# Performance work log

Hardware: AMD Instinct MI355X
Metric: run time of the kernel (lower is better)

Reference implementation:

```python
import jax, jax.numpy as jnp
import numpy as np

L, H, A, NREL2 = 3, 64, 64, 474
N_NODE, N_EDGE, B = 100000, 1000000, 32


def setup_inputs() -> dict:
    key = jax.random.key(0)
    ks = jax.random.split(key, 20)
    f = jax.random.normal
    s = 0.05
    return dict(
        sub_idx=jax.random.randint(ks[0], (N_EDGE,), 0, N_NODE),
        rel_idx=jax.random.randint(ks[1], (N_EDGE,), 0, NREL2),
        obj_idx=jax.random.randint(ks[2], (N_EDGE,), 0, N_NODE),
        edge_batch=jax.random.randint(ks[3], (N_EDGE,), 0, B),
        q_rel=jax.random.randint(ks[4], (B,), 0, NREL2),
        query_sub_idxs=jax.random.randint(ks[5], (B,), 0, N_NODE),
        rela_embed=f(ks[6], (L, NREL2, H)) * s,
        query_rela_embed=f(ks[7], (NREL2, H)) * s,
        Ws=f(ks[8], (L, H, A)) * s,
        Wr=f(ks[9], (L, H, A)) * s,
        Wqr=f(ks[10], (L, H, A)) * s,
        bqr=f(ks[11], (L, A)) * s,
        w_alpha=f(ks[12], (L, A)) * s,
        b_alpha=f(ks[13], (L,)) * s,
        W_h=f(ks[14], (L, H, H)) * s,
        gru_Wih=f(ks[15], (L, 3 * H, H)) * s,
        gru_Whh=f(ks[16], (L, 3 * H, H)) * s,
        gru_bih=f(ks[17], (L, 3 * H)) * s,
        gru_bhh=f(ks[18], (L, 3 * H)) * s,
        W_final=f(ks[19], (H,)) * s,
        n_node=N_NODE,
    )


def reference(sub_idx, rel_idx, obj_idx, edge_batch, q_rel, query_sub_idxs,
              rela_embed, query_rela_embed, Ws, Wr, Wqr, bqr, w_alpha, b_alpha,
              W_h, gru_Wih, gru_Whh, gru_bih, gru_bhh, W_final, n_node):
    # initializer='relation': seed query-subject nodes with query relation embedding
    hidden = jnp.zeros((n_node, H), jnp.float32).at[query_sub_idxs].set(query_rela_embed[q_rel])
    h0 = jnp.zeros((n_node, H), jnp.float32)  # GRU state

    for l in range(L):
        # ---- GNNLayer: gather -> attention MLP -> scatter-add ----
        hs = hidden[sub_idx]                       # [E, H]
        hr = rela_embed[l][rel_idx]                # [E, H]
        h_qr = rela_embed[l][q_rel][edge_batch]    # [E, H] query-rel emb per edge
        pre = jax.nn.relu(hs @ Ws[l] + hr @ Wr[l] + h_qr @ Wqr[l] + bqr[l])  # [E, A]
        alpha = jax.nn.sigmoid(pre @ w_alpha[l] + b_alpha[l])[:, None]       # [E, 1]
        msg = alpha * (hs * hr)                                              # [E, H]
        agg = jax.ops.segment_sum(msg, obj_idx, num_segments=n_node)        # [N, H]
        hidden = jax.nn.relu(agg @ W_h[l])

        # act_signal: mask untouched nodes (detached in original)
        mask = jnp.where(jax.lax.stop_gradient(jnp.sum(hidden, -1)) == 0, 0.0, 1.0)[:, None]

        # ---- one GRU step per node (PyTorch GRU math) ----
        gi = hidden @ gru_Wih[l].T + gru_bih[l]   # [N, 3H]
        gh = h0 @ gru_Whh[l].T + gru_bhh[l]       # [N, 3H]
        i_r, i_z, i_n = jnp.split(gi, 3, axis=-1)
        h_r, h_z, h_n = jnp.split(gh, 3, axis=-1)
        r = jax.nn.sigmoid(i_r + h_r)
        z = jax.nn.sigmoid(i_z + h_z)
        n = jnp.tanh(i_n + r * h_n)
        h_new = (1.0 - z) * n + z * h0
        hidden = h_new * mask
        h0 = h_new * mask

    # readout='linear', no bias
    scores = hidden @ W_final                     # [N]
    return scores
```

## Files before the change

kernel.cpp:

```cpp
#include <hip/hip_runtime.h>
#include <hip/hip_bf16.h>

#define NL 3
#define HD 64
#define TCAP 2048
#define NB 4

typedef unsigned char u8;

__device__ __forceinline__ float sigf(float x){ return 1.f/(1.f+__expf(-x)); }

__device__ __forceinline__ float wsum(float v){
  #pragma unroll
  for (int off=32; off; off>>=1) v += __shfl_xor(v, off, 64);
  return v;
}

__device__ __forceinline__ float bcastf(float v, int l){
  return __int_as_float(__builtin_amdgcn_readlane(__float_as_int(v), l));
}

__device__ __forceinline__ float ldin(const void* p, size_t i, int bf){
  return bf ? __bfloat162float(((const __hip_bfloat16*)p)[i]) : ((const float*)p)[i];
}

__global__ void k_dtype(const unsigned short* __restrict__ probe, int* __restrict__ flag){
  int lane = threadIdx.x & 63;
  unsigned short h = probe[lane];
  int e = (h >> 7) & 0xFF;
  int sane = ((h & 0x7FFF) == 0) || (e >= 96 && e <= 132);
  unsigned long long m = __ballot(sane != 0);
  if (lane == 0) flag[0] = (__popcll(m) >= 56) ? 1 : 0;
}

__global__ void k_prep(
    const void* __restrict__ W_h, const void* __restrict__ Ws,
    const void* __restrict__ Wih, const void* __restrict__ Whh,
    const void* __restrict__ bih, const void* __restrict__ bhh,
    const void* __restrict__ wal, const void* __restrict__ bal,
    const void* __restrict__ Wf,  const void* __restrict__ rel,
    float* __restrict__ WhF, float* __restrict__ WsF,
    float* __restrict__ WiT, float* __restrict__ WhT,
    float* __restrict__ biF, float* __restrict__ bhF,
    float* __restrict__ waF, float* __restrict__ baF,
    float* __restrict__ WfF, float* __restrict__ REL,
    const int* __restrict__ flag, int NR)
{
  int bf = flag[0];
  int j = blockIdx.x*256 + threadIdx.x;
  const int sWT = NL*HD*HD, sWI = NL*192*HD, sB = NL*192;
  if (j < sWT){ WhF[j]=ldin(W_h,j,bf); return; } j-=sWT;
  if (j < sWT){ WsF[j]=ldin(Ws ,j,bf); return; } j-=sWT;
  if (j < sWI){ int l=j/(192*HD), q=j%(192*HD), h=q/192, a=q%192;
                WiT[j]=ldin(Wih,(size_t)l*192*HD + (size_t)a*HD + h,bf); return; } j-=sWI;
  if (j < sWI){ int l=j/(192*HD), q=j%(192*HD), h=q/192, a=q%192;
                WhT[j]=ldin(Whh,(size_t)l*192*HD + (size_t)a*HD + h,bf); return; } j-=sWI;
  if (j < sB){ biF[j]=ldin(bih,j,bf); return; } j-=sB;
  if (j < sB){ bhF[j]=ldin(bhh,j,bf); return; } j-=sB;
  if (j < NL*HD){ waF[j]=ldin(wal,j,bf); return; } j-=NL*HD;
  if (j < NL){ baF[j]=ldin(bal,j,bf); return; } j-=NL;
  if (j < HD){ WfF[j]=ldin(Wf,j,bf); return; } j-=HD;
  if (j < NL*NR*HD){ REL[j]=ldin(rel,j,bf); return; }
}

__global__ void k_tables(
    const void* __restrict__ rel, const void* __restrict__ Wr,
    const void* __restrict__ Wqr, const void* __restrict__ bqr,
    const int* __restrict__ q_rel,
    float* __restrict__ R2, float* __restrict__ QR,
    const int* __restrict__ flag, int NR, int B)
{
  int bf = flag[0];
  int lane = threadIdx.x & 63;
  int bid = blockIdx.x;
  if (bid < NL*NR){
    int l = bid/NR, r = bid%NR;
    float x = ldin(rel,(size_t)(l*NR+r)*HD + lane,bf);
    float acc = 0.f;
    #pragma unroll
    for (int h=0; h<HD; ++h)
      acc = fmaf(bcastf(x, h), ldin(Wr,(size_t)(l*HD+h)*HD + lane,bf), acc);
    R2[(size_t)bid*HD + lane] = acc;
  } else {
    int b2 = bid - NL*NR;
    int l = b2/B, b = b2%B;
    int r = q_rel[b];
    float x = ldin(rel,(size_t)(l*NR+r)*HD + lane,bf);
    float acc = ldin(bqr,(size_t)l*HD + lane,bf);
    #pragma unroll
    for (int h=0; h<HD; ++h)
      acc = fmaf(bcastf(x, h), ldin(Wqr,(size_t)(l*HD+h)*HD + lane,bf), acc);
    QR[(size_t)b2*HD + lane] = acc;
  }
}

__global__ void k_init(
    const int* __restrict__ qsub, const int* __restrict__ q_rel,
    const void* __restrict__ qre, const float* __restrict__ WsF0,
    float* __restrict__ hid, float* __restrict__ HS2, u8* __restrict__ liveB,
    int* __restrict__ stamp, int* __restrict__ plist, int* __restrict__ pcnt,
    const int* __restrict__ flag, int B)
{
  int bf = flag[0];
  int lane = threadIdx.x & 63;
  int b = blockIdx.x;
  int n = qsub[b];
  for (int b2 = b+1; b2 < B; ++b2) if (qsub[b2] == n) return;
  int r = q_rel[b];
  float v = ldin(qre,(size_t)r*HD + lane,bf);
  hid[(size_t)n*HD + lane] = v;
  float acc = 0.f;
  #pragma unroll 8
  for (int h=0; h<HD; ++h)
    acc = fmaf(bcastf(v,h), WsF0[h*HD + lane], acc);
  HS2[(size_t)n*HD + lane] = acc;
  if (lane==0){
    liveB[n] = 1;
    stamp[n] = 1;
    int idx = atomicAdd(pcnt, 1);
    plist[idx] = n;
  }
}

__global__ void __launch_bounds__(256) k_edge(
    const int* __restrict__ sub, const int* __restrict__ rel_i,
    const int* __restrict__ obj, const int* __restrict__ eb,
    const u8* __restrict__ liveB,
    const float* __restrict__ hid, const float* __restrict__ HS2,
    const float* __restrict__ R2l, const float* __restrict__ QRl,
    const float* __restrict__ RELl, const float* __restrict__ waFl,
    const float* __restrict__ baFl, float* __restrict__ agg,
    int* __restrict__ stamp, int* __restrict__ tlist, int* __restrict__ tcnt,
    int ep, int E)
{
  __shared__ int s_cnt;
  __shared__ int s_base;
  __shared__ int s_buf[TCAP];
  if (threadIdx.x == 0) s_cnt = 0;
  __syncthreads();

  int lane = threadIdx.x & 63;
  int wid = (blockIdx.x*256 + threadIdx.x) >> 6;
  int nw = gridDim.x*4;
  float wa = waFl[lane];
  float ba = baFl[0];

  for (long long base = (long long)wid*64; base < E; base += (long long)nw*64){
    int e = (int)base + lane;
    int s = (e < E) ? sub[e] : 0;
    bool liv = (e < E) && (liveB[s] != 0);
    unsigned long long mask = __ballot(liv);
    while (mask){
      int bit = (int)__ffsll(mask) - 1;
      mask &= mask - 1;
      int ee = (int)base + bit;
      int ss = sub[ee], r = rel_i[ee], o = obj[ee], b = eb[ee];
      float hs  = hid[(size_t)ss*HD + lane];
      float pre = HS2[(size_t)ss*HD + lane] + R2l[(size_t)r*HD + lane] + QRl[(size_t)b*HD + lane];
      pre = fmaxf(pre, 0.f);
      float d = wsum(pre*wa) + ba;
      float alpha = sigf(d);
      float msg = alpha * hs * RELl[(size_t)r*HD + lane];
      unsafeAtomicAdd(&agg[(size_t)o*HD + lane], msg);
      if (lane==0){
        int old = atomicExch(&stamp[o], ep);
        if (old != ep){
          int li = atomicAdd(&s_cnt, 1);
          if (li < TCAP) s_buf[li] = o;
          else { int gi = atomicAdd(tcnt, 1); tlist[gi] = o; }
        }
      }
    }
  }

  __syncthreads();
  int cnt = s_cnt; if (cnt > TCAP) cnt = TCAP;
  if (threadIdx.x == 0 && cnt > 0) s_base = atomicAdd(tcnt, cnt);
  __syncthreads();
  if (cnt > 0){
    int b0 = s_base;
    for (int i = threadIdx.x; i < cnt; i += 256) tlist[b0 + i] = s_buf[i];
  }
}

__global__ void __launch_bounds__(256) k_node(
    const int* __restrict__ tlist, const int* __restrict__ tcnt,
    float* __restrict__ agg, float* __restrict__ hid, float* __restrict__ HS2,
    u8* __restrict__ liveB,
    const float* __restrict__ WhFl,
    const float* __restrict__ WiTl,
    const float* __restrict__ WhTl,
    const float* __restrict__ biFl, const float* __restrict__ bhFl,
    const float* __restrict__ WsFn,
    const float* __restrict__ WfF,
    float* __restrict__ out, int N, int isFirst, int isLast)
{
  int cntv = tcnt[0]; if (cntv > N) cntv = N;
  int lane = threadIdx.x & 63;
  int wid = (blockIdx.x*256 + threadIdx.x) >> 6;
  int nw = gridDim.x*4;
  float bi0=biFl[lane], bi1=biFl[HD+lane], bi2=biFl[2*HD+lane];
  float bh0=bhFl[lane], bh1=bhFl[HD+lane], bh2=bhFl[2*HD+lane];
  float wfv = isLast ? WfF[lane] : 0.f;

  for (int i0 = wid*NB; i0 < cntv; i0 += nw*NB){
    int nd[NB]; bool val[NB]; float av[NB];
    #pragma unroll
    for (int j=0;j<NB;++j){
      val[j] = (i0+j) < cntv;
      nd[j]  = tlist[val[j] ? (i0+j) : i0];
      av[j]  = val[j] ? agg[(size_t)nd[j]*HD + lane] : 0.f;
    }
    if (!isLast){
      #pragma unroll
      for (int j=0;j<NB;++j) if (val[j]) agg[(size_t)nd[j]*HD + lane] = 0.f;
    }

    float hm[NB] = {0.f,0.f,0.f,0.f};
    #pragma unroll 8
    for (int h=0; h<HD; ++h){
      float w = WhFl[h*HD + lane];
      #pragma unroll
      for (int j=0;j<NB;++j) hm[j] = fmaf(bcastf(av[j],h), w, hm[j]);
    }
    float mask[NB]; float h0v[NB];
    #pragma unroll
    for (int j=0;j<NB;++j){
      hm[j] = fmaxf(hm[j], 0.f);
      mask[j] = (__ballot(hm[j] != 0.f) != 0ull) ? 1.f : 0.f;
      h0v[j] = 0.f;
    }
    if (!isFirst){
      #pragma unroll
      for (int j=0;j<NB;++j){
        bool wl = val[j] && (liveB[nd[j]] != 0);
        float hv = hid[(size_t)nd[j]*HD + lane];
        h0v[j] = wl ? hv : 0.f;
      }
    }

    float gi0[NB], gi1[NB], gi2[NB], gh0[NB], gh1[NB], gh2[NB];
    #pragma unroll
    for (int j=0;j<NB;++j){ gi0[j]=bi0; gi1[j]=bi1; gi2[j]=bi2; gh0[j]=bh0; gh1[j]=bh1; gh2[j]=bh2; }
    #pragma unroll 4
    for (int h=0; h<HD; ++h){
      const float* __restrict__ wr = WiTl + (size_t)h*192;
      float w0 = wr[lane], w1 = wr[64+lane], w2 = wr[128+lane];
      #pragma unroll
      for (int j=0;j<NB;++j){
        float x = bcastf(hm[j],h);
        gi0[j] = fmaf(x, w0, gi0[j]);
        gi1[j] = fmaf(x, w1, gi1[j]);
        gi2[j] = fmaf(x, w2, gi2[j]);
      }
    }
    if (!isFirst){
      #pragma unroll 4
      for (int h=0; h<HD; ++h){
        const float* __restrict__ wr = WhTl + (size_t)h*192;
        float w0 = wr[lane], w1 = wr[64+lane], w2 = wr[128+lane];
        #pragma unroll
        for (int j=0;j<NB;++j){
          float y = bcastf(h0v[j],h);
          gh0[j] = fmaf(y, w0, gh0[j]);
          gh1[j] = fmaf(y, w1, gh1[j]);
          gh2[j] = fmaf(y, w2, gh2[j]);
        }
      }
    }

    float hn[NB];
    #pragma unroll
    for (int j=0;j<NB;++j){
      float r = sigf(gi0[j]+gh0[j]);
      float z = sigf(gi1[j]+gh1[j]);
      float nn = tanhf(gi2[j] + r*gh2[j]);
      hn[j] = ((1.f - z)*nn + z*h0v[j])*mask[j];
    }

    if (isLast){
      #pragma unroll
      for (int j=0;j<NB;++j){
        float sc = wsum(hn[j] * wfv);
        if (lane==0 && val[j]) out[nd[j]] = sc;
      }
      continue;
    }
    #pragma unroll
    for (int j=0;j<NB;++j){
      unsigned long long lv = __ballot(hn[j] != 0.f);
      if (val[j]){
        hid[(size_t)nd[j]*HD + lane] = hn[j];
        if (lane==0) liveB[nd[j]] = lv ? (u8)1 : (u8)0;
      }
    }

    float acc[NB] = {0.f,0.f,0.f,0.f};
    #pragma unroll 8
    for (int h=0; h<HD; ++h){
      float w = WsFn[h*HD + lane];
      #pragma unroll
      for (int j=0;j<NB;++j) acc[j] = fmaf(bcastf(hn[j],h), w, acc[j]);
    }
    #pragma unroll
    for (int j=0;j<NB;++j) if (val[j]) HS2[(size_t)nd[j]*HD + lane] = acc[j];
  }
}

__global__ void k_died(const int* __restrict__ plist, const int* __restrict__ pcnt,
                       const int* __restrict__ stamp, u8* __restrict__ liveB, int ep, int N)
{
  int cntv = pcnt[0]; if (cntv > N) cntv = N;
  int t = blockIdx.x*256 + threadIdx.x;
  for (int i = t; i < cntv; i += gridDim.x*256){
    int n = plist[i];
    if (stamp[n] != ep) liveB[n] = 0;
  }
}

extern "C" void kernel_launch(void* const* d_in, const int* in_sizes, int n_in,
                              void* d_out, int out_size, void* d_ws, size_t ws_size,
                              hipStream_t stream)
{
  const int* sub   = (const int*)d_in[0];
  const int* rel_i = (const int*)d_in[1];
  const int* obj   = (const int*)d_in[2];
  const int* eb    = (const int*)d_in[3];
  const int* q_rel = (const int*)d_in[4];
  const int* qsub  = (const int*)d_in[5];
  const void* rela = d_in[6];
  const void* qre  = d_in[7];
  const void* Wsp  = d_in[8];
  const void* Wr   = d_in[9];
  const void* Wqr  = d_in[10];
  const void* bqr  = d_in[11];
  const void* wal  = d_in[12];
  const void* bal  = d_in[13];
  const void* W_h  = d_in[14];
  const void* Wih  = d_in[15];
  const void* Whh  = d_in[16];
  const void* bih  = d_in[17];
  const void* bhh  = d_in[18];
  const void* Wf   = d_in[19];

  int E  = in_sizes[0];
  int B  = in_sizes[4];
  int NR = in_sizes[6]/(NL*HD);
  int N  = out_size;

  float* ws = (float*)d_ws;
  size_t o = 0;
  float* agg  = ws + o; o += (size_t)N*HD;
  float* hid  = ws + o; o += (size_t)N*HD;
  float* HS2  = ws + o; o += (size_t)N*HD;
  float* R2   = ws + o; o += (size_t)NL*NR*HD;
  float* QR   = ws + o; o += (size_t)NL*B*HD;
  float* REL  = ws + o; o += (size_t)NL*NR*HD;
  float* WhF  = ws + o; o += NL*HD*HD;
  float* WsF  = ws + o; o += NL*HD*HD;
  float* WiT  = ws + o; o += NL*192*HD;
  float* WhT  = ws + o; o += NL*192*HD;
  float* biF  = ws + o; o += NL*192;
  float* bhF  = ws + o; o += NL*192;
  float* waF  = ws + o; o += NL*HD;
  float* baF  = ws + o; o += NL;
  float* WfF  = ws + o; o += HD;
  int*   listA= (int*)(ws + o); o += N;
  int*   listB= (int*)(ws + o); o += N;
  int*   stamp= (int*)(ws + o); o += N;
  int*   cnts = (int*)(ws + o); o += 16;
  u8*    liveB= (u8*)(ws + o);

  hipMemsetAsync(agg,   0, (size_t)N*HD*sizeof(float), stream);
  hipMemsetAsync(stamp, 0, (size_t)N*sizeof(int) + 16*sizeof(int) + (size_t)N, stream);
  hipMemsetAsync(d_out, 0, (size_t)N*sizeof(float), stream);

  k_dtype<<<1, 64, 0, stream>>>((const unsigned short*)rela, cnts+8);

  int prepN = 2*(NL*HD*HD) + 2*(NL*192*HD) + 2*(NL*192) + NL*HD + NL + HD + NL*NR*HD;
  k_prep<<<(prepN+255)/256, 256, 0, stream>>>(W_h, Wsp, Wih, Whh, bih, bhh, wal, bal, Wf, rela,
      WhF, WsF, WiT, WhT, biF, bhF, waF, baF, WfF, REL, cnts+8, NR);
  k_tables<<<NL*NR + NL*B, 64, 0, stream>>>(rela, Wr, Wqr, bqr, q_rel, R2, QR, cnts+8, NR, B);
  k_init<<<B, 64, 0, stream>>>(qsub, q_rel, qre, WsF, hid, HS2, liveB,
                               stamp, listA, cnts+3, cnts+8, B);

  int* curT = listB;
  int* prevL = listA;
  for (int l=0; l<NL; ++l){
    int ep = l + 2;
    k_edge<<<1024, 256, 0, stream>>>(sub, rel_i, obj, eb, liveB, hid, HS2,
        R2 + (size_t)l*NR*HD, QR + (size_t)l*B*HD, REL + (size_t)l*NR*HD,
        waF + l*HD, baF + l, agg, stamp, curT, cnts+4+l, ep, E);
    k_node<<<2048, 256, 0, stream>>>(curT, cnts+4+l, agg, hid, HS2, liveB,
        WhF + (size_t)l*HD*HD, WiT + (size_t)l*192*HD, WhT + (size_t)l*192*HD,
        biF + l*192, bhF + l*192,
        (l < NL-1) ? (WsF + (size_t)(l+1)*HD*HD) : WsF,
        WfF, (float*)d_out, N, (l==0)?1:0, (l==NL-1)?1:0);
    if (l < NL-1){
      k_died<<<64, 256, 0, stream>>>(prevL, (l==0) ? (cnts+3) : (cnts+4+l-1),
                                     stamp, liveB, ep, N);
    }
    int* t = prevL; prevL = curT; curT = t;
  }
}
```

Measured before the change: 197.4 us.

## Pack node liveness into a bitmask and double node batch per wave

Replaces the per-node byte liveness array with a 32-bit-word bitmask, updated through atomicOr/atomicAnd. The edge kernel's random liveness lookups then touch a 12.5KB array that fits in cache, instead of a 100KB byte array. Separately, the node kernel processes 8 nodes per wave instead of 4 to reuse weight loads across more nodes. The larger batch raises register pressure and leaves fewer waves for the small live-node counts, and the atomic bit updates add cost in k_node and k_died.

```diff
diff --git a/kernel.cpp b/kernel.cpp
--- a/kernel.cpp
+++ b/kernel.cpp
@@ -4,7 +4,7 @@
 #define NL 3
 #define HD 64
 #define TCAP 2048
-#define NB 4
+#define NB 8
 
 typedef unsigned char u8;
 
@@ -97,7 +97,7 @@
 __global__ void k_init(
     const int* __restrict__ qsub, const int* __restrict__ q_rel,
     const void* __restrict__ qre, const float* __restrict__ WsF0,
-    float* __restrict__ hid, float* __restrict__ HS2, u8* __restrict__ liveB,
+    float* __restrict__ hid, float* __restrict__ HS2, unsigned* __restrict__ liveW,
     int* __restrict__ stamp, int* __restrict__ plist, int* __restrict__ pcnt,
     const int* __restrict__ flag, int B)
 {
@@ -115,7 +115,7 @@
     acc = fmaf(bcastf(v,h), WsF0[h*HD + lane], acc);
   HS2[(size_t)n*HD + lane] = acc;
   if (lane==0){
-    liveB[n] = 1;
+    atomicOr(&liveW[n>>5], 1u<<(n&31));
     stamp[n] = 1;
     int idx = atomicAdd(pcnt, 1);
     plist[idx] = n;
@@ -125,7 +125,7 @@
 __global__ void __launch_bounds__(256) k_edge(
     const int* __restrict__ sub, const int* __restrict__ rel_i,
     const int* __restrict__ obj, const int* __restrict__ eb,
-    const u8* __restrict__ liveB,
+    const unsigned* __restrict__ liveW,
     const float* __restrict__ hid, const float* __restrict__ HS2,
     const float* __restrict__ R2l, const float* __restrict__ QRl,
     const float* __restrict__ RELl, const float* __restrict__ waFl,
@@ -148,7 +148,8 @@
   for (long long base = (long long)wid*64; base < E; base += (long long)nw*64){
     int e = (int)base + lane;
     int s = (e < E) ? sub[e] : 0;
-    bool liv = (e < E) && (liveB[s] != 0);
+    unsigned w = liveW[s>>5];
+    bool liv = (e < E) && ((w >> (s&31)) & 1u);
     unsigned long long mask = __ballot(liv);
     while (mask){
       int bit = (int)__ffsll(mask) - 1;
@@ -186,7 +187,7 @@
 __global__ void __launch_bounds__(256) k_node(
     const int* __restrict__ tlist, const int* __restrict__ tcnt,
     float* __restrict__ agg, float* __restrict__ hid, float* __restrict__ HS2,
-    u8* __restrict__ liveB,
+    unsigned* __restrict__ liveW,
     const float* __restrict__ WhFl,
     const float* __restrict__ WiTl,
     const float* __restrict__ WhTl,
@@ -216,7 +217,9 @@
       for (int j=0;j<NB;++j) if (val[j]) agg[(size_t)nd[j]*HD + lane] = 0.f;
     }
 
-    float hm[NB] = {0.f,0.f,0.f,0.f};
+    float hm[NB];
+    #pragma unroll
+    for (int j=0;j<NB;++j) hm[j] = 0.f;
     #pragma unroll 8
     for (int h=0; h<HD; ++h){
       float w = WhFl[h*HD + lane];
@@ -233,7 +236,7 @@
     if (!isFirst){
       #pragma unroll
       for (int j=0;j<NB;++j){
-        bool wl = val[j] && (liveB[nd[j]] != 0);
+        bool wl = val[j] && ((liveW[nd[j]>>5] >> (nd[j]&31)) & 1u);
         float hv = hid[(size_t)nd[j]*HD + lane];
         h0v[j] = wl ? hv : 0.f;
       }
@@ -291,11 +294,17 @@
       unsigned long long lv = __ballot(hn[j] != 0.f);
       if (val[j]){
         hid[(size_t)nd[j]*HD + lane] = hn[j];
-        if (lane==0) liveB[nd[j]] = lv ? (u8)1 : (u8)0;
-      }
-    }
-
-    float acc[NB] = {0.f,0.f,0.f,0.f};
+        if (lane==0){
+          unsigned bit = 1u << (nd[j]&31);
+          if (lv) atomicOr (&liveW[nd[j]>>5],  bit);
+          else    atomicAnd(&liveW[nd[j]>>5], ~bit);
+        }
+      }
+    }
+
+    float acc[NB];
+    #pragma unroll
+    for (int j=0;j<NB;++j) acc[j] = 0.f;
     #pragma unroll 8
     for (int h=0; h<HD; ++h){
       float w = WsFn[h*HD + lane];
@@ -308,13 +317,14 @@
 }
 
 __global__ void k_died(const int* __restrict__ plist, const int* __restrict__ pcnt,
-                       const int* __restrict__ stamp, u8* __restrict__ liveB, int ep, int N)
+                       const int* __restrict__ stamp, unsigned* __restrict__ liveW,
+                       int ep, int N)
 {
   int cntv = pcnt[0]; if (cntv > N) cntv = N;
   int t = blockIdx.x*256 + threadIdx.x;
   for (int i = t; i < cntv; i += gridDim.x*256){
     int n = plist[i];
-    if (stamp[n] != ep) liveB[n] = 0;
+    if (stamp[n] != ep) atomicAnd(&liveW[n>>5], ~(1u<<(n&31)));
   }
 }
 
@@ -347,6 +357,7 @@
   int B  = in_sizes[4];
   int NR = in_sizes[6]/(NL*HD);
   int N  = out_size;
+  int NW = (N + 31) / 32;
 
   float* ws = (float*)d_ws;
   size_t o = 0;
@@ -369,10 +380,10 @@
   int*   listB= (int*)(ws + o); o += N;
   int*   stamp= (int*)(ws + o); o += N;
   int*   cnts = (int*)(ws + o); o += 16;
-  u8*    liveB= (u8*)(ws + o);
+  unsigned* liveW = (unsigned*)(ws + o);
 
   hipMemsetAsync(agg,   0, (size_t)N*HD*sizeof(float), stream);
-  hipMemsetAsync(stamp, 0, (size_t)N*sizeof(int) + 16*sizeof(int) + (size_t)N, stream);
+  hipMemsetAsync(stamp, 0, (size_t)N*sizeof(int) + 16*sizeof(int) + (size_t)NW*sizeof(unsigned), stream);
   hipMemsetAsync(d_out, 0, (size_t)N*sizeof(float), stream);
 
   k_dtype<<<1, 64, 0, stream>>>((const unsigned short*)rela, cnts+8);
@@ -381,24 +392,24 @@
   k_prep<<<(prepN+255)/256, 256, 0, stream>>>(W_h, Wsp, Wih, Whh, bih, bhh, wal, bal, Wf, rela,
       WhF, WsF, WiT, WhT, biF, bhF, waF, baF, WfF, REL, cnts+8, NR);
   k_tables<<<NL*NR + NL*B, 64, 0, stream>>>(rela, Wr, Wqr, bqr, q_rel, R2, QR, cnts+8, NR, B);
-  k_init<<<B, 64, 0, stream>>>(qsub, q_rel, qre, WsF, hid, HS2, liveB,
+  k_init<<<B, 64, 0, stream>>>(qsub, q_rel, qre, WsF, hid, HS2, liveW,
                                stamp, listA, cnts+3, cnts+8, B);
 
   int* curT = listB;
   int* prevL = listA;
   for (int l=0; l<NL; ++l){
     int ep = l + 2;
-    k_edge<<<1024, 256, 0, stream>>>(sub, rel_i, obj, eb, liveB, hid, HS2,
+    k_edge<<<1024, 256, 0, stream>>>(sub, rel_i, obj, eb, liveW, hid, HS2,
         R2 + (size_t)l*NR*HD, QR + (size_t)l*B*HD, REL + (size_t)l*NR*HD,
         waF + l*HD, baF + l, agg, stamp, curT, cnts+4+l, ep, E);
-    k_node<<<2048, 256, 0, stream>>>(curT, cnts+4+l, agg, hid, HS2, liveB,
+    k_node<<<2048, 256, 0, stream>>>(curT, cnts+4+l, agg, hid, HS2, liveW,
         WhF + (size_t)l*HD*HD, WiT + (size_t)l*192*HD, WhT + (size_t)l*192*HD,
         biF + l*192, bhF + l*192,
         (l < NL-1) ? (WsF + (size_t)(l+1)*HD*HD) : WsF,
         WfF, (float*)d_out, N, (l==0)?1:0, (l==NL-1)?1:0);
     if (l < NL-1){
       k_died<<<64, 256, 0, stream>>>(prevL, (l==0) ? (cnts+3) : (cnts+4+l-1),
-                                     stamp, liveB, ep, N);
+                                     stamp, liveW, ep, N);
     }
     int* t = prevL; prevL = curT; curT = t;
   }
```

New measurement: 220.6 us. 11.7% more time.

## Vectorize edge liveness scan, skip hidden-GRU matvec for dead nodes, raise NB to 8

Applied to the files above, without the earlier changes.

The edge kernel now has each wave handle 256 edges, loading subject indices as int4 and building four liveness ballots per step, which cuts per-edge scan overhead. In the node kernel the Whh matvec runs only for nodes whose previous state is live, instead of for every node whenever the layer is not the first. The number of nodes per wave goes from 4 to 8 to reuse weight loads more. The per-node conditional matvec reloads the weights for each node and raises register pressure, which could lower occupancy.

```diff
diff --git a/kernel.cpp b/kernel.cpp
--- a/kernel.cpp
+++ b/kernel.cpp
@@ -4,7 +4,7 @@
 #define NL 3
 #define HD 64
 #define TCAP 2048
-#define NB 4
+#define NB 8
 
 typedef unsigned char u8;
 
@@ -145,29 +145,46 @@
   float wa = waFl[lane];
   float ba = baFl[0];
 
-  for (long long base = (long long)wid*64; base < E; base += (long long)nw*64){
-    int e = (int)base + lane;
-    int s = (e < E) ? sub[e] : 0;
-    bool liv = (e < E) && (liveB[s] != 0);
-    unsigned long long mask = __ballot(liv);
-    while (mask){
-      int bit = (int)__ffsll(mask) - 1;
-      mask &= mask - 1;
-      int ee = (int)base + bit;
-      int ss = sub[ee], r = rel_i[ee], o = obj[ee], b = eb[ee];
-      float hs  = hid[(size_t)ss*HD + lane];
-      float pre = HS2[(size_t)ss*HD + lane] + R2l[(size_t)r*HD + lane] + QRl[(size_t)b*HD + lane];
-      pre = fmaxf(pre, 0.f);
-      float d = wsum(pre*wa) + ba;
-      float alpha = sigf(d);
-      float msg = alpha * hs * RELl[(size_t)r*HD + lane];
-      unsafeAtomicAdd(&agg[(size_t)o*HD + lane], msg);
-      if (lane==0){
-        int old = atomicExch(&stamp[o], ep);
-        if (old != ep){
-          int li = atomicAdd(&s_cnt, 1);
-          if (li < TCAP) s_buf[li] = o;
-          else { int gi = atomicAdd(tcnt, 1); tlist[gi] = o; }
+  for (long long base = (long long)wid*256; base < E; base += (long long)nw*256){
+    unsigned long long m[4];
+    if (base + 256 <= E){
+      int4 s4 = *reinterpret_cast<const int4*>(&sub[base + 4*(long long)lane]);
+      bool l0 = liveB[s4.x] != 0;
+      bool l1 = liveB[s4.y] != 0;
+      bool l2 = liveB[s4.z] != 0;
+      bool l3 = liveB[s4.w] != 0;
+      m[0] = __ballot(l0); m[1] = __ballot(l1);
+      m[2] = __ballot(l2); m[3] = __ballot(l3);
+    } else {
+      #pragma unroll
+      for (int j=0;j<4;++j){
+        long long e = base + 4*(long long)lane + j;
+        bool lv = (e < E) && (liveB[sub[e]] != 0);
+        m[j] = __ballot(lv);
+      }
+    }
+    #pragma unroll
+    for (int j=0;j<4;++j){
+      unsigned long long mask = m[j];
+      while (mask){
+        int bit = (int)__ffsll(mask) - 1;
+        mask &= mask - 1;
+        long long ee = base + 4*(long long)bit + j;
+        int ss = sub[ee], r = rel_i[ee], o = obj[ee], b = eb[ee];
+        float hs  = hid[(size_t)ss*HD + lane];
+        float pre = HS2[(size_t)ss*HD + lane] + R2l[(size_t)r*HD + lane] + QRl[(size_t)b*HD + lane];
+        pre = fmaxf(pre, 0.f);
+        float d = wsum(pre*wa) + ba;
+        float alpha = sigf(d);
+        float msg = alpha * hs * RELl[(size_t)r*HD + lane];
+        unsafeAtomicAdd(&agg[(size_t)o*HD + lane], msg);
+        if (lane==0){
+          int old = atomicExch(&stamp[o], ep);
+          if (old != ep){
+            int li = atomicAdd(&s_cnt, 1);
+            if (li < TCAP) s_buf[li] = o;
+            else { int gi = atomicAdd(tcnt, 1); tlist[gi] = o; }
+          }
         }
       }
     }
@@ -204,11 +221,12 @@
   float wfv = isLast ? WfF[lane] : 0.f;
 
   for (int i0 = wid*NB; i0 < cntv; i0 += nw*NB){
-    int nd[NB]; bool val[NB]; float av[NB];
+    int nd[NB]; bool val[NB]; bool wp[NB]; float av[NB];
     #pragma unroll
     for (int j=0;j<NB;++j){
       val[j] = (i0+j) < cntv;
       nd[j]  = tlist[val[j] ? (i0+j) : i0];
+      wp[j]  = (!isFirst) && val[j] && (liveB[nd[j]] != 0);
       av[j]  = val[j] ? agg[(size_t)nd[j]*HD + lane] : 0.f;
     }
     if (!isLast){
@@ -216,7 +234,9 @@
       for (int j=0;j<NB;++j) if (val[j]) agg[(size_t)nd[j]*HD + lane] = 0.f;
     }
 
-    float hm[NB] = {0.f,0.f,0.f,0.f};
+    float hm[NB];
+    #pragma unroll
+    for (int j=0;j<NB;++j) hm[j] = 0.f;
     #pragma unroll 8
     for (int h=0; h<HD; ++h){
       float w = WhFl[h*HD + lane];
@@ -228,15 +248,7 @@
     for (int j=0;j<NB;++j){
       hm[j] = fmaxf(hm[j], 0.f);
       mask[j] = (__ballot(hm[j] != 0.f) != 0ull) ? 1.f : 0.f;
-      h0v[j] = 0.f;
-    }
-    if (!isFirst){
-      #pragma unroll
-      for (int j=0;j<NB;++j){
-        bool wl = val[j] && (liveB[nd[j]] != 0);
-        float hv = hid[(size_t)nd[j]*HD + lane];
-        h0v[j] = wl ? hv : 0.f;
-      }
+      h0v[j] = wp[j] ? hid[(size_t)nd[j]*HD + lane] : 0.f;
     }
 
     float gi0[NB], gi1[NB], gi2[NB], gh0[NB], gh1[NB], gh2[NB];
@@ -254,17 +266,16 @@
         gi2[j] = fmaf(x, w2, gi2[j]);
       }
     }
-    if (!isFirst){
-      #pragma unroll 4
-      for (int h=0; h<HD; ++h){
-        const float* __restrict__ wr = WhTl + (size_t)h*192;
-        float w0 = wr[lane], w1 = wr[64+lane], w2 = wr[128+lane];
-        #pragma unroll
-        for (int j=0;j<NB;++j){
+    #pragma unroll
+    for (int j=0;j<NB;++j){
+      if (wp[j]){
+        #pragma unroll 4
+        for (int h=0; h<HD; ++h){
+          const float* __restrict__ wr = WhTl + (size_t)h*192;
           float y = bcastf(h0v[j],h);
-          gh0[j] = fmaf(y, w0, gh0[j]);
-          gh1[j] = fmaf(y, w1, gh1[j]);
-          gh2[j] = fmaf(y, w2, gh2[j]);
+          gh0[j] = fmaf(y, wr[lane],     gh0[j]);
+          gh1[j] = fmaf(y, wr[64+lane],  gh1[j]);
+          gh2[j] = fmaf(y, wr[128+lane], gh2[j]);
         }
       }
     }
@@ -295,7 +306,9 @@
       }
     }
 
-    float acc[NB] = {0.f,0.f,0.f,0.f};
+    float acc[NB];
+    #pragma unroll
+    for (int j=0;j<NB;++j) acc[j] = 0.f;
     #pragma unroll 8
     for (int h=0; h<HD; ++h){
       float w = WsFn[h*HD + lane];
```

After: 188.1 us. -4.7%, faster.
